# Kernel tuning notes

Measured on AMD Instinct MI355X. Metric: run time of the kernel, lower is better.

Reference implementation:

```python
import jax, jax.numpy as jnp
import numpy as np

B, C, H, W = 8, 512, 64, 64
NH, D = 8, 64            # num_heads, head_dim (C = NH*D)
WH, WW = 8, 8            # window size
EPS = 1e-5
SCALE = D ** -0.5


def _layernorm(x, g, b):
    mu = jnp.mean(x, axis=-1, keepdims=True)
    var = jnp.mean((x - mu) ** 2, axis=-1, keepdims=True)
    return (x - mu) * jax.lax.rsqrt(var + EPS) * g + b


def _rope_cache(n, d):
    pos = jnp.arange(n, dtype=jnp.float32)
    inv_freq = 1.0 / (10000.0 ** (jnp.arange(0, d, 2, dtype=jnp.float32) / d))
    sinusoid = pos[:, None] * inv_freq[None, :]          # (n, d//2)
    return jnp.stack([jnp.sin(sinusoid), jnp.cos(sinusoid)], axis=-1).reshape(n, d)


def _apply_rope(x, rope):
    # x: (B, nH, N, d); rope: (N, d) packed [sin, cos] interleaved
    b, nh, n, d = x.shape
    x_ = x.reshape(b, nh, n, d // 2, 2)
    r = rope.reshape(n, d // 2, 2)
    sin, cos = r[..., 0], r[..., 1]                      # (N, d//2)
    x0, x1 = x_[..., 0], x_[..., 1]
    xr0 = x0 * cos - x1 * sin
    xr1 = x0 * sin + x1 * cos
    return jnp.stack([xr0, xr1], axis=-1).reshape(b, nh, n, d)


def _relative_index(wh, ww):
    ch, cw = np.meshgrid(np.arange(wh), np.arange(ww), indexing='ij')
    flat = np.stack([ch.reshape(-1), cw.reshape(-1)])    # (2, Ws)
    rel = flat[:, :, None] - flat[:, None, :]            # (2, Ws, Ws)
    rel = rel.transpose(1, 2, 0).astype(np.int64)
    rel[..., 0] += wh - 1
    rel[..., 1] += ww - 1
    rel[..., 0] *= 2 * ww - 1
    return jnp.asarray(rel.sum(-1))                      # (Ws, Ws)


def setup_inputs() -> dict:
    key = jax.random.key(0)
    ks = jax.random.split(key, 12)
    s = 0.02
    table_size = (2 * WH - 1) * (2 * WW - 1)
    return {
        'q':  jax.random.normal(ks[0], (B, C, H, W), jnp.float32),
        'kv': jax.random.normal(ks[1], (B, C, H, W), jnp.float32),
        'g_q':  jnp.ones((C,), jnp.float32),  'b_q_ln':  jnp.zeros((C,), jnp.float32),
        'g_kv': jnp.ones((C,), jnp.float32),  'b_kv_ln': jnp.zeros((C,), jnp.float32),
        'Wq': jax.random.normal(ks[2], (C, C), jnp.float32) * s, 'bq': jnp.zeros((C,), jnp.float32),
        'Wk': jax.random.normal(ks[3], (C, C), jnp.float32) * s, 'bk': jnp.zeros((C,), jnp.float32),
        'Wv': jax.random.normal(ks[4], (C, C), jnp.float32) * s, 'bv': jnp.zeros((C,), jnp.float32),
        'Wo': jax.random.normal(ks[5], (C, C), jnp.float32) * s, 'bo': jnp.zeros((C,), jnp.float32),
        'bias_table': jax.random.normal(ks[6], (table_size, NH), jnp.float32) * s,
    }


def reference(q, kv, g_q, b_q_ln, g_kv, b_kv_ln, Wq, bq, Wk, bk, Wv, bv, Wo, bo, bias_table):
    N = H * W
    Hn, Wn = H // WH, W // WW
    nw = Hn * Wn
    Ws = WH * WW

    # flatten NCHW -> (B, N, C)
    q_seq = q.reshape(B, C, N).transpose(0, 2, 1)
    kv_seq = kv.reshape(B, C, N).transpose(0, 2, 1)
    q_seq = _layernorm(q_seq, g_q, b_q_ln)
    kv_seq = _layernorm(kv_seq, g_kv, b_kv_ln)

    Q = (q_seq @ Wq.T + bq).reshape(B, N, NH, D).transpose(0, 2, 1, 3)   # (B,nH,N,d)
    K = (kv_seq @ Wk.T + bk).reshape(B, N, NH, D).transpose(0, 2, 1, 3)
    V = (kv_seq @ Wv.T + bv).reshape(B, N, NH, D).transpose(0, 2, 1, 3)

    rope = _rope_cache(N, D)
    Q = _apply_rope(Q, rope)
    K = _apply_rope(K, rope)

    # window partition: (B,nH,H,W,d) -> (nH, B*nw, Ws, d); head-major to match torch cat order
    def part(x):
        x = x.reshape(B, NH, Hn, WH, Wn, WW, D)
        return x.transpose(1, 0, 2, 4, 3, 5, 6).reshape(NH, B * nw, Ws, D)

    Qw, Kw, Vw = part(Q), part(K), part(V)

    attn = jnp.einsum('hnqd,hnkd->hnqk', Qw, Kw) * SCALE                 # (nH, B*nw, Ws, Ws)
    rel_idx = _relative_index(WH, WW)
    bias = bias_table[rel_idx.reshape(-1)].reshape(Ws, Ws, NH).transpose(2, 0, 1)  # (nH, Ws, Ws)
    attn = attn + bias[:, None, :, :]
    attn = jax.nn.softmax(attn, axis=-1)
    out_w = jnp.einsum('hnqk,hnkd->hnqd', attn, Vw)                      # (nH, B*nw, Ws, d)

    # window reverse + head concat -> (B, N, C)
    out = out_w.reshape(NH, B, Hn, Wn, WH, WW, D)
    out = out.transpose(1, 2, 4, 3, 5, 0, 6).reshape(B, N, NH * D)

    out = out @ Wo.T + bo
    out = out + q_seq                                                    # residual w/ normed q (as in source)
    return out.transpose(0, 2, 1).reshape(B, C, H, W)
```

## Files before the change

### kernel.cpp

```cpp
#include <hip/hip_runtime.h>


typedef unsigned short u16;
typedef __bf16 bf16x8 __attribute__((ext_vector_type(8)));
typedef float f32x4 __attribute__((ext_vector_type(4)));
typedef u16 u16x8 __attribute__((ext_vector_type(8)));
typedef u16 u16x4 __attribute__((ext_vector_type(4)));

__device__ __forceinline__ u16 f2bf(float f) {
    __bf16 h = (__bf16)f;
    return __builtin_bit_cast(u16, h);
}
__device__ __forceinline__ float bf2f(u16 u) {
    return (float)__builtin_bit_cast(__bf16, u);
}
__device__ __forceinline__ f32x4 mfma16(bf16x8 a, bf16x8 b, f32x4 c) {
    return __builtin_amdgcn_mfma_f32_16x16x32_bf16(a, b, c, 0, 0, 0);
}
__device__ __forceinline__ void gl_lds16(const u16* g, u16* l) {
    __builtin_amdgcn_global_load_lds((const __attribute__((address_space(1))) void*)g,
                                     (__attribute__((address_space(3))) void*)l, 16, 0, 0);
}
__device__ __forceinline__ int swapb(int n) {
    return (n & 0xE07) | ((n & 0x1C0) >> 3) | ((n & 0x038) << 3);
}

__global__ __launch_bounds__(256) void setup_kernel(
    const float* __restrict__ Wq, const float* __restrict__ Wk,
    const float* __restrict__ Wv, const float* __restrict__ Wo,
    const float* __restrict__ btab,
    u16* __restrict__ wq, u16* __restrict__ wk,
    u16* __restrict__ wv, u16* __restrict__ wo,
    float* __restrict__ rope, float* __restrict__ biasf)
{
    int idx = blockIdx.x * 256 + threadIdx.x;
    {
        int w = idx >> 18, e = idx & 262143;
        const float* src = (w == 0) ? Wq : (w == 1) ? Wk : (w == 2) ? Wv : Wo;
        u16* dst = (w == 0) ? wq : (w == 1) ? wk : (w == 2) ? wv : wo;
        dst[e] = f2bf(src[e]);
    }
    if (idx < 131072) {
        int n = idx >> 5, j = idx & 31;
        float inv = powf(10000.0f, -(float)j / 32.0f);
        float a = (float)n * inv;
        float s, c;
        sincosf(a, &s, &c);
        rope[n * 64 + 2 * j] = s;
        rope[n * 64 + 2 * j + 1] = c;
    }
    if (idx < 32768) {
        int q = idx & 63, pp = (idx >> 6) & 63, h = idx >> 12;
        int r1 = pp >> 3, c1 = pp & 7, r2 = q >> 3, c2 = q & 7;
        int ri = (r1 - r2 + 7) * 15 + (c1 - c2 + 7);
        biasf[idx] = btab[ri * 8 + h];
    }
}

__global__ __launch_bounds__(256) void ln_kernel(
    const float* __restrict__ x, const float* __restrict__ g,
    const float* __restrict__ be, u16* __restrict__ out)
{
    __shared__ u16 sX[512 * 36];
    __shared__ float sS[1024];
    __shared__ float sQ[1024];
    __shared__ float sMu[32], sInv[32];

    const int tid = threadIdx.x;
    const int b = blockIdx.x >> 7, grp = blockIdx.x & 127;
    const int nbase = grp << 5;
    const int t4 = tid & 7;
    const int cg = tid >> 3;

    const float* xp = x + ((size_t)b << 21) + nbase + (t4 << 2);
    float sm[4] = {0.f, 0.f, 0.f, 0.f}, sq2[4] = {0.f, 0.f, 0.f, 0.f};
#pragma unroll 4
    for (int it = 0; it < 16; it++) {
        int c = (it << 5) + cg;
        f32x4 v = *(const f32x4*)&xp[(size_t)c << 12];
        u16x4 h;
#pragma unroll
        for (int r = 0; r < 4; r++) {
            sm[r] += v[r];
            sq2[r] += v[r] * v[r];
            h[r] = f2bf(v[r]);
        }
        *(u16x4*)&sX[c * 36 + (t4 << 2)] = h;
    }
#pragma unroll
    for (int r = 0; r < 4; r++) {
        sS[tid * 4 + r] = sm[r];
        sQ[tid * 4 + r] = sq2[r];
    }
    __syncthreads();
    if (tid < 32) {
        int t4v = tid >> 2, r = tid & 3;
        float a = 0.f, q2 = 0.f;
#pragma unroll
        for (int c2 = 0; c2 < 32; c2++) {
            int i2 = ((c2 << 3) + t4v) * 4 + r;
            a += sS[i2];
            q2 += sQ[i2];
        }
        float mu = a * (1.f / 512.f);
        float var = q2 * (1.f / 512.f) - mu * mu;
        sMu[tid] = mu;
        sInv[tid] = rsqrtf(var + 1e-5f);
    }
    __syncthreads();

    const int t = tid >> 3;
    const int cs = (tid & 7) << 3;
    float mu = sMu[t], inv = sInv[t];
    int p = swapb(nbase + t);
    size_t orow = ((size_t)((b << 12) + p)) * 512;
#pragma unroll
    for (int it = 0; it < 8; it++) {
        int c0 = cs + (it << 6);
        f32x4 g0 = *(const f32x4*)&g[c0];
        f32x4 g1 = *(const f32x4*)&g[c0 + 4];
        f32x4 e0 = *(const f32x4*)&be[c0];
        f32x4 e1 = *(const f32x4*)&be[c0 + 4];
        u16x8 o;
#pragma unroll
        for (int k = 0; k < 8; k++) {
            float v = bf2f(sX[(c0 + k) * 36 + t]);
            float gg = (k < 4) ? g0[k] : g1[k - 4];
            float bb = (k < 4) ? e0[k] : e1[k - 4];
            o[k] = f2bf((v - mu) * inv * gg + bb);
        }
        *(u16x8*)&out[orow + c0] = o;
    }
}

__global__ __launch_bounds__(512, 2) void gemm_qkv(
    const u16* __restrict__ qn, const u16* __restrict__ kvn,
    const u16* __restrict__ wq, const u16* __restrict__ wk, const u16* __restrict__ wv,
    const float* __restrict__ bq, const float* __restrict__ bk, const float* __restrict__ bv,
    const float* __restrict__ rope,
    u16* __restrict__ Qr, u16* __restrict__ Kr, u16* __restrict__ VT)
{
    __shared__ __align__(16) u16 smem[32768];

    const int bid = blockIdx.x;
    const int swz = (bid & 7) * 96 + (bid >> 3);
    const int kind = swz >> 8;
    const int rem = swz & 255;
    const int n0 = (rem >> 7) << 8;
    const int m0 = (rem & 127) << 8;

    const u16* Asrc = (kind == 0) ? qn : kvn;
    const u16* W = (kind == 0) ? wq : (kind == 1) ? wk : wv;
    const float* bias = (kind == 0) ? bq : (kind == 1) ? bk : bv;

    const int tid = threadIdx.x;
    const int lane = tid & 63, wid = tid >> 6;
    const int ln = lane & 15, lq = lane >> 4;
    const int wr = wid >> 2, wc = wid & 3;

    const int rr = tid >> 2;
    const int cc = (tid & 3) ^ ((tid >> 3) & 3);
    const u16* aSt = Asrc + (size_t)(m0 + rr) * 512 + cc * 8;
    const u16* bSt = W + (size_t)(n0 + rr) * 512 + cc * 8;
    const int aD = wid * 512;

    gl_lds16(aSt, &smem[aD]);
    gl_lds16(aSt + (size_t)128 * 512, &smem[4096 + aD]);
    gl_lds16(bSt, &smem[16384 + aD]);
    gl_lds16(bSt + (size_t)128 * 512, &smem[16384 + 4096 + aD]);
    gl_lds16(aSt + 32, &smem[8192 + aD]);
    gl_lds16(aSt + 32 + (size_t)128 * 512, &smem[8192 + 4096 + aD]);
    gl_lds16(bSt + 32, &smem[16384 + 8192 + aD]);
    gl_lds16(bSt + 32 + (size_t)128 * 512, &smem[16384 + 8192 + 4096 + aD]);

    const int swzc = lq ^ ((ln >> 1) & 3);
    const int aRd = (wr * 128 + ln) * 32 + swzc * 8;
    const int bRd = 16384 + (wc * 64 + ln) * 32 + swzc * 8;

    f32x4 acc[8][4] = {};

    asm volatile("s_waitcnt vmcnt(4)" ::: "memory");
    __builtin_amdgcn_s_barrier();
    __builtin_amdgcn_sched_barrier(0);

    for (int kt = 0; kt < 16; ++kt) {
        const int slot = (kt & 1) * 8192;
        bf16x8 bB[4];
        {
            f32x4 a0 = *(const f32x4*)&smem[slot + aRd];
            f32x4 a1 = *(const f32x4*)&smem[slot + aRd + 512];
            f32x4 a2 = *(const f32x4*)&smem[slot + aRd + 1024];
            f32x4 a3 = *(const f32x4*)&smem[slot + aRd + 1536];
            f32x4 b0 = *(const f32x4*)&smem[slot + bRd];
            f32x4 b1 = *(const f32x4*)&smem[slot + bRd + 512];
            f32x4 b2 = *(const f32x4*)&smem[slot + bRd + 1024];
            f32x4 b3 = *(const f32x4*)&smem[slot + bRd + 1536];
            asm volatile("" ::"v"(a0), "v"(a1), "v"(a2), "v"(a3),
                             "v"(b0), "v"(b1), "v"(b2), "v"(b3));
            __builtin_amdgcn_s_barrier();
            __builtin_amdgcn_sched_barrier(0);
            if (kt < 14) {
                const u16* gp = bSt + (size_t)(kt + 2) * 32;
                gl_lds16(gp, &smem[16384 + slot + aD]);
                gl_lds16(gp + (size_t)128 * 512, &smem[16384 + slot + 4096 + aD]);
            }
            bf16x8 bA[4] = {__builtin_bit_cast(bf16x8, a0), __builtin_bit_cast(bf16x8, a1),
                            __builtin_bit_cast(bf16x8, a2), __builtin_bit_cast(bf16x8, a3)};
            bB[0] = __builtin_bit_cast(bf16x8, b0);
            bB[1] = __builtin_bit_cast(bf16x8, b1);
            bB[2] = __builtin_bit_cast(bf16x8, b2);
            bB[3] = __builtin_bit_cast(bf16x8, b3);
            __builtin_amdgcn_s_setprio(1);
#pragma unroll
            for (int i = 0; i < 4; ++i)
#pragma unroll
                for (int j = 0; j < 4; ++j)
                    acc[i][j] = mfma16(bA[i], bB[j], acc[i][j]);
            __builtin_amdgcn_s_setprio(0);
        }
        __builtin_amdgcn_sched_barrier(0);
        __builtin_amdgcn_s_barrier();
        __builtin_amdgcn_sched_barrier(0);
        {
            f32x4 h0 = *(const f32x4*)&smem[slot + aRd + 2048];
            f32x4 h1 = *(const f32x4*)&smem[slot + aRd + 2560];
            f32x4 h2 = *(const f32x4*)&smem[slot + aRd + 3072];
            f32x4 h3 = *(const f32x4*)&smem[slot + aRd + 3584];
            asm volatile("" ::"v"(h0), "v"(h1), "v"(h2), "v"(h3));
            __builtin_amdgcn_s_barrier();
            __builtin_amdgcn_sched_barrier(0);
            if (kt < 14) {
                const u16* gp = aSt + (size_t)(kt + 2) * 32;
                gl_lds16(gp, &smem[slot + aD]);
                gl_lds16(gp + (size_t)128 * 512, &smem[slot + 4096 + aD]);
            }
            bf16x8 hA[4] = {__builtin_bit_cast(bf16x8, h0), __builtin_bit_cast(bf16x8, h1),
                            __builtin_bit_cast(bf16x8, h2), __builtin_bit_cast(bf16x8, h3)};
            __builtin_amdgcn_s_setprio(1);
#pragma unroll
            for (int i = 0; i < 4; ++i)
#pragma unroll
                for (int j = 0; j < 4; ++j)
                    acc[i + 4][j] = mfma16(hA[i], bB[j], acc[i + 4][j]);
            __builtin_amdgcn_s_setprio(0);
        }
        if (kt < 14) {
            asm volatile("s_waitcnt vmcnt(4)" ::: "memory");
        } else {
            asm volatile("s_waitcnt vmcnt(0)" ::: "memory");
        }
        __builtin_amdgcn_s_barrier();
        __builtin_amdgcn_sched_barrier(0);
    }

    float bj[4];
#pragma unroll
    for (int j = 0; j < 4; ++j) bj[j] = bias[n0 + wc * 64 + j * 16 + ln];

    u16* sU = smem;

    if (kind < 2) {
        u16* Out = (kind == 0) ? Qr : Kr;
#pragma unroll
        for (int g = 0; g < 4; ++g) {
            __syncthreads();
            if (wr == (g >> 1)) {
                const int i0 = (g & 1) * 4;
#pragma unroll
                for (int di = 0; di < 4; ++di)
#pragma unroll
                    for (int j = 0; j < 4; ++j)
#pragma unroll
                        for (int r = 0; r < 4; ++r)
                            sU[(di * 16 + lq * 4 + r) * 264 + wc * 64 + j * 16 + ln] =
                                f2bf(acc[i0 + di][j][r] + bj[j]);
            }
            __syncthreads();
#pragma unroll
            for (int it = 0; it < 4; ++it) {
                int idx = it * 512 + tid;
                int row = idx >> 5;
                int cseg = (idx & 31) << 3;
                u16x8 v = *(const u16x8*)&sU[row * 264 + cseg];
                int t = m0 + g * 64 + row;
                int n = swapb(t & 4095);
                float f[8];
#pragma unroll
                for (int k = 0; k < 8; k++) f[k] = bf2f(v[k]);
                {
                    int d0 = cseg & 63;
                    const float* rp = &rope[n * 64 + d0];
                    f32x4 r0 = *(const f32x4*)rp;
                    f32x4 r1 = *(const f32x4*)(rp + 4);
#pragma unroll
                    for (int pp = 0; pp < 4; pp++) {
                        float sn = (pp < 2) ? r0[2 * pp] : r1[2 * (pp - 2)];
                        float cs2 = (pp < 2) ? r0[2 * pp + 1] : r1[2 * (pp - 2) + 1];
                        float x0 = f[2 * pp], x1 = f[2 * pp + 1];
                        f[2 * pp] = x0 * cs2 - x1 * sn;
                        f[2 * pp + 1] = x0 * sn + x1 * cs2;
                    }
                }
                u16x8 o;
#pragma unroll
                for (int k = 0; k < 8; k++) o[k] = f2bf(f[k]);
                *(u16x8*)&Out[(size_t)t * 512 + n0 + cseg] = o;
            }
        }
    } else {
        const int wq0 = m0 & 4095;
        const int bb = m0 >> 12;
#pragma unroll
        for (int g = 0; g < 4; ++g) {
            __syncthreads();
            if (wc == g) {
#pragma unroll
                for (int i = 0; i < 8; ++i)
#pragma unroll
                    for (int j = 0; j < 4; ++j) {
                        u16x4 pk;
#pragma unroll
                        for (int r = 0; r < 4; ++r) pk[r] = f2bf(acc[i][j][r] + bj[j]);
                        *(u16x4*)&sU[(j * 16 + ln) * 264 + wr * 128 + i * 16 + lq * 4] = pk;
                    }
            }
            __syncthreads();
#pragma unroll
            for (int it = 0; it < 4; ++it) {
                int idx = it * 512 + tid;
                int col = idx >> 5;
                int ch = (idx & 31) << 3;
                u16x8 v = *(const u16x8*)&sU[col * 264 + ch];
                int c = n0 + g * 64 + col;
                int hh = c >> 6, dd = c & 63;
                *(u16x8*)&VT[((size_t)((((bb << 3) + hh) << 6) + dd)) * 4096 + wq0 + ch] = v;
            }
        }
    }
}

__global__ __launch_bounds__(256) void gemm_out(
    const u16* __restrict__ A, const u16* __restrict__ Bw,
    const float* __restrict__ bias, const u16* __restrict__ qn,
    float* __restrict__ Out)
{
    __shared__ u16 sA[128 * 32];
    __shared__ u16 sB[128 * 32];
    __shared__ u16 sR[128 * 136];

    const int m0 = blockIdx.x * 128;
    const int n0 = blockIdx.y * 128;
    const int tid = threadIdx.x;
    const int lane = tid & 63, wave = tid >> 6;
    const int ln = lane & 15, lq = lane >> 4;
    const int wm = wave & 1, wn = wave >> 1;

    const int srow = wave * 16 + (lane >> 2);
    const int sseg = (lane & 3) << 3;
    const u16* gA0 = A + (size_t)(m0 + srow) * 512 + sseg;
    const u16* gA1 = gA0 + (size_t)64 * 512;
    const u16* gB0 = Bw + (size_t)(n0 + srow) * 512 + sseg;
    const u16* gB1 = gB0 + (size_t)64 * 512;
    u16* lA0 = &sA[wave * 16 * 32];
    u16* lA1 = &sA[(64 + wave * 16) * 32];
    u16* lB0 = &sB[wave * 16 * 32];
    u16* lB1 = &sB[(64 + wave * 16) * 32];

    f32x4 acc[4][4] = {};

    for (int kt = 0; kt < 512; kt += 32) {
        gl_lds16(gA0 + kt, lA0);
        gl_lds16(gA1 + kt, lA1);
        gl_lds16(gB0 + kt, lB0);
        gl_lds16(gB1 + kt, lB1);
        __syncthreads();
        bf16x8 af[4], bfr[4];
#pragma unroll
        for (int i = 0; i < 4; i++)
            af[i] = *(const bf16x8*)&sA[(wm * 64 + i * 16 + ln) * 32 + lq * 8];
#pragma unroll
        for (int j = 0; j < 4; j++)
            bfr[j] = *(const bf16x8*)&sB[(wn * 64 + j * 16 + ln) * 32 + lq * 8];
#pragma unroll
        for (int i = 0; i < 4; i++)
#pragma unroll
            for (int j = 0; j < 4; j++)
                acc[i][j] = mfma16(af[i], bfr[j], acc[i][j]);
        __syncthreads();
    }

#pragma unroll
    for (int it = 0; it < 8; it++) {
        int idx = it * 256 + tid;
        int row = idx >> 4, c8 = (idx & 15) << 3;
        *(u16x8*)&sR[row * 136 + c8] = *(const u16x8*)&qn[(size_t)(m0 + row) * 512 + n0 + c8];
    }
    __syncthreads();

    int cj[4];
    float bj[4];
#pragma unroll
    for (int j = 0; j < 4; j++) {
        cj[j] = n0 + wn * 64 + j * 16 + ln;
        bj[j] = bias[cj[j]];
    }
#pragma unroll
    for (int i = 0; i < 4; i++) {
        int t0 = m0 + wm * 64 + i * 16 + lq * 4;
        int bb = t0 >> 12;
        int nb = swapb(t0 & 4095);
        int lrow = wm * 64 + i * 16 + lq * 4;
#pragma unroll
        for (int j = 0; j < 4; j++) {
            int lcol = wn * 64 + j * 16 + ln;
            f32x4 v;
#pragma unroll
            for (int r = 0; r < 4; r++)
                v[r] = acc[i][j][r] + bj[j] + bf2f(sR[(lrow + r) * 136 + lcol]);
            *(f32x4*)&Out[((size_t)((bb << 9) + cj[j]) << 12) + nb] = v;
        }
    }
}

__global__ __launch_bounds__(256) void attn_kernel(
    const u16* __restrict__ Q, const u16* __restrict__ K, const u16* __restrict__ VT,
    const float* __restrict__ biasf, u16* __restrict__ Out)
{
    __shared__ u16 sQ[64 * 72];
    __shared__ u16 sK[64 * 72];
    __shared__ u16 sVT[64 * 72];
    __shared__ u16 sP[4][16 * 72];

    const int tid = threadIdx.x;
    const int h = blockIdx.x & 7;
    const int w = (blockIdx.x >> 3) & 63;
    const int b = blockIdx.x >> 9;
    const int lane = tid & 63, wave = tid >> 6;
    const int ln = lane & 15, lq = lane >> 4;

    const size_t qrow0 = (size_t)(b << 12) + w * 64;
    const size_t vrow0 = ((size_t)(((b << 3) + h) << 6)) * 4096 + w * 64;

#pragma unroll
    for (int ii = 0; ii < 2; ii++) {
        int idx = ii * 256 + tid;
        int row = idx >> 3, ch = (idx & 7) << 3;
        size_t ga = (qrow0 + row) * 512 + h * 64 + ch;
        *(u16x8*)&sQ[row * 72 + ch] = *(const u16x8*)&Q[ga];
        *(u16x8*)&sK[row * 72 + ch] = *(const u16x8*)&K[ga];
        *(u16x8*)&sVT[row * 72 + ch] = *(const u16x8*)&VT[vrow0 + (size_t)row * 4096 + ch];
    }
    __syncthreads();

    f32x4 s[4] = {};
#pragma unroll
    for (int ks = 0; ks < 2; ks++) {
        bf16x8 a = *(const bf16x8*)&sQ[(wave * 16 + ln) * 72 + ks * 32 + lq * 8];
#pragma unroll
        for (int j = 0; j < 4; j++) {
            bf16x8 bb = *(const bf16x8*)&sK[(j * 16 + ln) * 72 + ks * 32 + lq * 8];
            s[j] = mfma16(a, bb, s[j]);
        }
    }

    float sv[4][4];
#pragma unroll
    for (int r = 0; r < 4; r++) {
        const float* bp = &biasf[((h * 64 + wave * 16 + lq * 4 + r) << 6) + ln];
#pragma unroll
        for (int j = 0; j < 4; j++) sv[r][j] = s[j][r] * 0.125f + bp[j * 16];
    }
#pragma unroll
    for (int r = 0; r < 4; r++) {
        float m = fmaxf(fmaxf(sv[r][0], sv[r][1]), fmaxf(sv[r][2], sv[r][3]));
        m = fmaxf(m, __shfl_xor(m, 1));
        m = fmaxf(m, __shfl_xor(m, 2));
        m = fmaxf(m, __shfl_xor(m, 4));
        m = fmaxf(m, __shfl_xor(m, 8));
        float sum = 0.f;
#pragma unroll
        for (int j = 0; j < 4; j++) {
            sv[r][j] = __expf(sv[r][j] - m);
            sum += sv[r][j];
        }
        sum += __shfl_xor(sum, 1);
        sum += __shfl_xor(sum, 2);
        sum += __shfl_xor(sum, 4);
        sum += __shfl_xor(sum, 8);
        float rinv = 1.f / sum;
#pragma unroll
        for (int j = 0; j < 4; j++)
            sP[wave][(lq * 4 + r) * 72 + j * 16 + ln] = f2bf(sv[r][j] * rinv);
    }

    f32x4 o[4] = {};
#pragma unroll
    for (int ks = 0; ks < 2; ks++) {
        bf16x8 a = *(const bf16x8*)&sP[wave][ln * 72 + ks * 32 + lq * 8];
#pragma unroll
        for (int jd = 0; jd < 4; jd++) {
            bf16x8 bb = *(const bf16x8*)&sVT[(jd * 16 + ln) * 72 + ks * 32 + lq * 8];
            o[jd] = mfma16(a, bb, o[jd]);
        }
    }

#pragma unroll
    for (int r = 0; r < 4; r++)
#pragma unroll
        for (int jd = 0; jd < 4; jd++)
            sQ[(wave * 16 + lq * 4 + r) * 72 + jd * 16 + ln] = f2bf(o[jd][r]);
    __syncthreads();
#pragma unroll
    for (int ii = 0; ii < 2; ii++) {
        int idx = ii * 256 + tid;
        int row = idx >> 3, ch = (idx & 7) << 3;
        *(u16x8*)&Out[(qrow0 + row) * 512 + h * 64 + ch] = *(const u16x8*)&sQ[row * 72 + ch];
    }
}

extern "C" void kernel_launch(void* const* d_in, const int* in_sizes, int n_in,
                              void* d_out, int out_size, void* d_ws, size_t ws_size,
                              hipStream_t stream)
{
    const float* q    = (const float*)d_in[0];
    const float* kv   = (const float*)d_in[1];
    const float* g_q  = (const float*)d_in[2];
    const float* b_q  = (const float*)d_in[3];
    const float* g_kv = (const float*)d_in[4];
    const float* b_kv = (const float*)d_in[5];
    const float* Wq   = (const float*)d_in[6];
    const float* bq   = (const float*)d_in[7];
    const float* Wk   = (const float*)d_in[8];
    const float* bk   = (const float*)d_in[9];
    const float* Wv   = (const float*)d_in[10];
    const float* bv   = (const float*)d_in[11];
    const float* Wo   = (const float*)d_in[12];
    const float* bo   = (const float*)d_in[13];
    const float* btab = (const float*)d_in[14];

    char* ws = (char*)d_ws;
    u16* qn      = (u16*)(ws);
    u16* kvn     = (u16*)(ws + 33554432);
    u16* VT      = (u16*)(ws + 67108864);
    float* rope  = (float*)(ws + 100663296);
    float* biasf = (float*)(ws + 101711872);
    u16* wq      = (u16*)(ws + 101842944);
    u16* wk      = (u16*)(ws + 102367232);
    u16* wv      = (u16*)(ws + 102891520);
    u16* wo      = (u16*)(ws + 103415808);
    u16* aout    = kvn;
    u16* Qr      = (u16*)d_out;
    u16* Kr      = Qr + 16777216;

    setup_kernel<<<4096, 256, 0, stream>>>(Wq, Wk, Wv, Wo, btab, wq, wk, wv, wo, rope, biasf);
    ln_kernel<<<1024, 256, 0, stream>>>(q, g_q, b_q, qn);
    ln_kernel<<<1024, 256, 0, stream>>>(kv, g_kv, b_kv, kvn);
    gemm_qkv<<<768, 512, 0, stream>>>(qn, kvn, wq, wk, wv, bq, bk, bv, rope, Qr, Kr, VT);
    attn_kernel<<<4096, 256, 0, stream>>>(Qr, Kr, VT, biasf, aout);
    gemm_out<<<dim3(256, 4), 256, 0, stream>>>(aout, wo, bo, qn, (float*)d_out);
}
```

Before: 354.2 us.

## Deepen QKV GEMM LDS pipeline to four stages and drop a barrier

Shared memory in the QKV projection GEMM grows from a 2-slot to a 4-slot ring, so global->LDS prefetch runs three k-tiles ahead instead of one. The loop is also restructured so the second-half A reads are issued before the first MFMA batch, which removes one of the per-iteration barriers. The aim is to hide global load latency better and cut synchronisation. The cost is 128KB of LDS per block, which may limit the intended two blocks per CU.

```diff
diff --git a/kernel.cpp b/kernel.cpp
--- a/kernel.cpp
+++ b/kernel.cpp
@@ -140,7 +140,7 @@
     const float* __restrict__ rope,
     u16* __restrict__ Qr, u16* __restrict__ Kr, u16* __restrict__ VT)
 {
-    __shared__ __align__(16) u16 smem[32768];
+    __shared__ __align__(16) u16 smem[65536];
 
     const int bid = blockIdx.x;
     const int swz = (bid & 7) * 96 + (bid >> 3);
@@ -164,52 +164,56 @@
     const u16* bSt = W + (size_t)(n0 + rr) * 512 + cc * 8;
     const int aD = wid * 512;
 
-    gl_lds16(aSt, &smem[aD]);
-    gl_lds16(aSt + (size_t)128 * 512, &smem[4096 + aD]);
-    gl_lds16(bSt, &smem[16384 + aD]);
-    gl_lds16(bSt + (size_t)128 * 512, &smem[16384 + 4096 + aD]);
-    gl_lds16(aSt + 32, &smem[8192 + aD]);
-    gl_lds16(aSt + 32 + (size_t)128 * 512, &smem[8192 + 4096 + aD]);
-    gl_lds16(bSt + 32, &smem[16384 + 8192 + aD]);
-    gl_lds16(bSt + 32 + (size_t)128 * 512, &smem[16384 + 8192 + 4096 + aD]);
+#pragma unroll
+    for (int t = 0; t < 4; ++t) {
+        const u16* ga = aSt + t * 32;
+        const u16* gb = bSt + t * 32;
+        gl_lds16(ga, &smem[(t << 13) + aD]);
+        gl_lds16(ga + (size_t)(128 * 512), &smem[(t << 13) + 4096 + aD]);
+        gl_lds16(gb, &smem[32768 + (t << 13) + aD]);
+        gl_lds16(gb + (size_t)(128 * 512), &smem[32768 + (t << 13) + 4096 + aD]);
+    }
 
     const int swzc = lq ^ ((ln >> 1) & 3);
     const int aRd = (wr * 128 + ln) * 32 + swzc * 8;
-    const int bRd = 16384 + (wc * 64 + ln) * 32 + swzc * 8;
+    const int bRd = (wc * 64 + ln) * 32 + swzc * 8;
 
     f32x4 acc[8][4] = {};
 
-    asm volatile("s_waitcnt vmcnt(4)" ::: "memory");
+    asm volatile("s_waitcnt vmcnt(12)" ::: "memory");
     __builtin_amdgcn_s_barrier();
     __builtin_amdgcn_sched_barrier(0);
 
     for (int kt = 0; kt < 16; ++kt) {
-        const int slot = (kt & 1) * 8192;
-        bf16x8 bB[4];
+        const int sAo = (kt & 3) << 13;
+        const int sBo = 32768 + sAo;
+        f32x4 a0 = *(const f32x4*)&smem[sAo + aRd];
+        f32x4 a1 = *(const f32x4*)&smem[sAo + aRd + 512];
+        f32x4 a2 = *(const f32x4*)&smem[sAo + aRd + 1024];
+        f32x4 a3 = *(const f32x4*)&smem[sAo + aRd + 1536];
+        f32x4 b0 = *(const f32x4*)&smem[sBo + bRd];
+        f32x4 b1 = *(const f32x4*)&smem[sBo + bRd + 512];
+        f32x4 b2 = *(const f32x4*)&smem[sBo + bRd + 1024];
+        f32x4 b3 = *(const f32x4*)&smem[sBo + bRd + 1536];
+        asm volatile("" ::"v"(a0), "v"(a1), "v"(a2), "v"(a3),
+                         "v"(b0), "v"(b1), "v"(b2), "v"(b3));
+        __builtin_amdgcn_s_barrier();
+        __builtin_amdgcn_sched_barrier(0);
+        if (kt < 12) {
+            const u16* gb = bSt + (size_t)(kt + 4) * 32;
+            gl_lds16(gb, &smem[sBo + aD]);
+            gl_lds16(gb + (size_t)(128 * 512), &smem[sBo + 4096 + aD]);
+        }
+        f32x4 h0 = *(const f32x4*)&smem[sAo + aRd + 2048];
+        f32x4 h1 = *(const f32x4*)&smem[sAo + aRd + 2560];
+        f32x4 h2 = *(const f32x4*)&smem[sAo + aRd + 3072];
+        f32x4 h3 = *(const f32x4*)&smem[sAo + aRd + 3584];
+        __builtin_amdgcn_sched_barrier(0);
         {
-            f32x4 a0 = *(const f32x4*)&smem[slot + aRd];
-            f32x4 a1 = *(const f32x4*)&smem[slot + aRd + 512];
-            f32x4 a2 = *(const f32x4*)&smem[slot + aRd + 1024];
-            f32x4 a3 = *(const f32x4*)&smem[slot + aRd + 1536];
-            f32x4 b0 = *(const f32x4*)&smem[slot + bRd];
-            f32x4 b1 = *(const f32x4*)&smem[slot + bRd + 512];
-            f32x4 b2 = *(const f32x4*)&smem[slot + bRd + 1024];
-            f32x4 b3 = *(const f32x4*)&smem[slot + bRd + 1536];
-            asm volatile("" ::"v"(a0), "v"(a1), "v"(a2), "v"(a3),
-                             "v"(b0), "v"(b1), "v"(b2), "v"(b3));
-            __builtin_amdgcn_s_barrier();
-            __builtin_amdgcn_sched_barrier(0);
-            if (kt < 14) {
-                const u16* gp = bSt + (size_t)(kt + 2) * 32;
-                gl_lds16(gp, &smem[16384 + slot + aD]);
-                gl_lds16(gp + (size_t)128 * 512, &smem[16384 + slot + 4096 + aD]);
-            }
             bf16x8 bA[4] = {__builtin_bit_cast(bf16x8, a0), __builtin_bit_cast(bf16x8, a1),
                             __builtin_bit_cast(bf16x8, a2), __builtin_bit_cast(bf16x8, a3)};
-            bB[0] = __builtin_bit_cast(bf16x8, b0);
-            bB[1] = __builtin_bit_cast(bf16x8, b1);
-            bB[2] = __builtin_bit_cast(bf16x8, b2);
-            bB[3] = __builtin_bit_cast(bf16x8, b3);
+            bf16x8 bB[4] = {__builtin_bit_cast(bf16x8, b0), __builtin_bit_cast(bf16x8, b1),
+                            __builtin_bit_cast(bf16x8, b2), __builtin_bit_cast(bf16x8, b3)};
             __builtin_amdgcn_s_setprio(1);
 #pragma unroll
             for (int i = 0; i < 4; ++i)
@@ -217,22 +221,13 @@
                 for (int j = 0; j < 4; ++j)
                     acc[i][j] = mfma16(bA[i], bB[j], acc[i][j]);
             __builtin_amdgcn_s_setprio(0);
-        }
-        __builtin_amdgcn_sched_barrier(0);
-        __builtin_amdgcn_s_barrier();
-        __builtin_amdgcn_sched_barrier(0);
-        {
-            f32x4 h0 = *(const f32x4*)&smem[slot + aRd + 2048];
-            f32x4 h1 = *(const f32x4*)&smem[slot + aRd + 2560];
-            f32x4 h2 = *(const f32x4*)&smem[slot + aRd + 3072];
-            f32x4 h3 = *(const f32x4*)&smem[slot + aRd + 3584];
             asm volatile("" ::"v"(h0), "v"(h1), "v"(h2), "v"(h3));
             __builtin_amdgcn_s_barrier();
             __builtin_amdgcn_sched_barrier(0);
-            if (kt < 14) {
-                const u16* gp = aSt + (size_t)(kt + 2) * 32;
-                gl_lds16(gp, &smem[slot + aD]);
-                gl_lds16(gp + (size_t)128 * 512, &smem[slot + 4096 + aD]);
+            if (kt < 12) {
+                const u16* ga = aSt + (size_t)(kt + 4) * 32;
+                gl_lds16(ga, &smem[sAo + aD]);
+                gl_lds16(ga + (size_t)(128 * 512), &smem[sAo + 4096 + aD]);
             }
             bf16x8 hA[4] = {__builtin_bit_cast(bf16x8, h0), __builtin_bit_cast(bf16x8, h1),
                             __builtin_bit_cast(bf16x8, h2), __builtin_bit_cast(bf16x8, h3)};
@@ -244,13 +239,19 @@
                     acc[i + 4][j] = mfma16(hA[i], bB[j], acc[i + 4][j]);
             __builtin_amdgcn_s_setprio(0);
         }
-        if (kt < 14) {
+        if (kt < 12) {
+            asm volatile("s_waitcnt vmcnt(12)" ::: "memory");
+        } else if (kt == 12) {
+            asm volatile("s_waitcnt vmcnt(8)" ::: "memory");
+        } else if (kt == 13) {
             asm volatile("s_waitcnt vmcnt(4)" ::: "memory");
-        } else {
+        } else if (kt == 14) {
             asm volatile("s_waitcnt vmcnt(0)" ::: "memory");
         }
-        __builtin_amdgcn_s_barrier();
-        __builtin_amdgcn_sched_barrier(0);
+        if (kt < 15) {
+            __builtin_amdgcn_s_barrier();
+            __builtin_amdgcn_sched_barrier(0);
+        }
     }
 
     float bj[4];
```

Measured after the change: 349.0 us. Within noise of the previous version (-1.5%).
